# Kernel optimization log

Measured on AMD Instinct MI355X. Metric: run time of the kernel, lower is better.

## Reference

```python
import jax, jax.numpy as jnp
import numpy as np
from jax import lax

# dims
BS, C, H, W = 16, 684, 32, 128   # batch, encoder channels, feature-map H/W
Q, K, PAD = 256, 11, 5           # coverage channels, conv_Q kernel, padding
N, NP = 256, 512                 # decoder hidden n, attention dim n_prime
T = 4                            # prior attention steps stored in alpha


def setup_inputs() -> dict:
    key = jax.random.key(0)
    ks = jax.random.split(key, 10)
    s = 0.02  # small init scale (stand-in for xavier)
    return {
        "x": jax.random.normal(ks[0], (BS, C, H, W), jnp.float32),
        "st_hat": jax.random.normal(ks[1], (BS, 1, N), jnp.float32),
        "alpha": jax.random.uniform(ks[2], (BS, T, H * W), jnp.float32),
        # conv_Q: Conv2d(1, Q, k=11, pad=5)
        "convQ_w": jax.random.normal(ks[3], (Q, 1, K, K), jnp.float32) * s,
        "convQ_b": jnp.zeros((Q,), jnp.float32),
        # fc_Wa: Linear(n, n_prime)
        "Wa_w": jax.random.normal(ks[4], (NP, N), jnp.float32) * s,
        "Wa_b": jnp.zeros((NP,), jnp.float32),
        # conv_Ua: Conv2d(C, n_prime, k=1)
        "convUa_w": jax.random.normal(ks[5], (NP, C, 1, 1), jnp.float32) * s,
        "convUa_b": jnp.zeros((NP,), jnp.float32),
        # fc_Uf: Linear(Q, n_prime)
        "Uf_w": jax.random.normal(ks[6], (NP, Q), jnp.float32) * s,
        "Uf_b": jnp.zeros((NP,), jnp.float32),
        # fc_Va: Linear(n_prime, 1)
        "Va_w": jax.random.normal(ks[7], (1, NP), jnp.float32) * s,
        "Va_b": jnp.zeros((1,), jnp.float32),
    }


def reference(x, st_hat, alpha, convQ_w, convQ_b, Wa_w, Wa_b,
              convUa_w, convUa_b, Uf_w, Uf_b, Va_w, Va_b):
    bs, c, h, w = x.shape
    # beta: sum of past attention maps -> [bs, 1, h, w]
    beta = alpha.sum(axis=1).reshape(bs, 1, h, w)
    # conv_Q: coverage features [bs, Q, h, w]
    Fc = lax.conv_general_dilated(
        beta, convQ_w, window_strides=(1, 1), padding=[(PAD, PAD), (PAD, PAD)],
        dimension_numbers=("NCHW", "OIHW", "NCHW")) + convQ_b[None, :, None, None]
    # fc_Uf over channel dim after permute(2,3,0,1): [h, w, bs, n_prime]
    cover = jnp.einsum("bqhw,pq->hwbp", Fc, Uf_w) + Uf_b
    # conv_Ua (1x1 conv == per-pixel linear): [h, w, bs, n_prime]
    key = jnp.einsum("bchw,pc->hwbp", x, convUa_w[:, :, 0, 0]) + convUa_b
    # fc_Wa(st_hat).squeeze(1): [bs, n_prime]
    query = st_hat[:, 0, :] @ Wa_w.T + Wa_b
    # additive attention score
    score = jnp.tanh(key + query[None, None, :, :] + cover)  # [h,w,bs,np]
    # fc_Va -> e_t, permuted to [bs, h*w] (row-major over h,w like torch view)
    e = jnp.einsum("hwbp,p->bhw", score, Va_w[0]) + Va_b[0]
    e = e.reshape(bs, h * w)
    # softmax with the module's explicit exp/sum + eps formulation
    e_exp = jnp.exp(e)
    alpha_t = e_exp / (e_exp.sum(axis=1, keepdims=True) + 1e-8)  # [bs, hw]
    # context vector g_t = sum_n alpha_t[b,n] * x[b,c,n]
    context = jnp.einsum("bn,bcn->bc", alpha_t, x.reshape(bs, c, h * w))
    return context, alpha_t.reshape(bs, 1, h, w)
```

## Files before the change

### kernel.cpp

```cpp
#include <hip/hip_runtime.h>
#include <math.h>

#define BS 16
#define C_ 684
#define Hh 32
#define Ww 128
#define HW 4096
#define Qc 256
#define NP 512
#define Nn 256
#define NKT 26
#define NB 64

#define WS_BETA 0
#define WS_BIAS 65536
#define WS_EEXP 73728
#define WS_ESUM 139264
#define WS_ASW  139280

typedef __attribute__((ext_vector_type(8))) short bf16x8;
typedef __attribute__((ext_vector_type(4))) float f32x4;

static __device__ __forceinline__ short f2bf(float f) {
    unsigned u = __builtin_bit_cast(unsigned, f);
    u += 0x7fff + ((u >> 16) & 1);
    return (short)(u >> 16);
}

static __device__ __forceinline__ float fast_tanh(float v) {
    float ax = fabsf(v);
    float t = __expf(-2.f * ax);
    float th = (1.f - t) * __builtin_amdgcn_rcpf(1.f + t);
    return copysignf(th, v);
}

__global__ void k_prep(const float* __restrict__ alpha, const float* __restrict__ ua,
                       const float* __restrict__ ufw, const float* __restrict__ qw,
                       const float* __restrict__ st, const float* __restrict__ waw,
                       const float* __restrict__ wab, const float* __restrict__ ufb,
                       const float* __restrict__ qb, const float* __restrict__ uab,
                       float* __restrict__ beta, short* __restrict__ a_sw,
                       float* __restrict__ bias, float* __restrict__ esum) {
    int part = blockIdx.x, tid = threadIdx.x;
    if (part < 256) {
        int idx = part * 256 + tid;
        int b = idx >> 12, n = idx & 4095;
        const float* a = alpha + (size_t)b * 4 * HW + n;
        beta[idx] = a[0] + a[HW] + a[2 * HW] + a[3 * HW];
    } else if (part < 1920) {
        int idx = (part - 256) * 256 + tid;
        int j = idx & 7, m = (idx >> 3) & 511, g = (idx >> 12) & 3, kt = idx >> 14;
        int k = kt * 32 + g * 8 + j;
        float v = 0.f;
        if (k < C_) {
            v = ua[m * C_ + k];
        } else if (k < C_ + 121) {
            int tap = k - C_;
            const float* ur = ufw + m * Qc;
            float s = 0.f;
            for (int q = 0; q < Qc; ++q) s += ur[q] * qw[q * 121 + tap];
            v = s;
        }
        a_sw[idx] = f2bf(v);
    } else if (part < 1952) {
        int idx = (part - 1920) * 256 + tid;
        int b = idx >> 9, p = idx & 511;
        float s = wab[p] + ufb[p] + uab[p];
        const float* sv = st + b * Nn;
        const float* wr = waw + p * Nn;
        for (int n = 0; n < Nn; ++n) s += sv[n] * wr[n];
        const float* ur = ufw + p * Qc;
        for (int q = 0; q < Qc; ++q) s += ur[q] * qb[q];
        bias[idx] = s;
    } else {
        if (tid < BS) esum[tid] = 0.f;
    }
}

__launch_bounds__(256, 2)
__global__ void k_gemm(const short* __restrict__ a_sw, const float* __restrict__ x,
                       const float* __restrict__ beta, const float* __restrict__ bias,
                       const float* __restrict__ vaw, const float* __restrict__ vab,
                       float* __restrict__ eexp, float* __restrict__ esum) {
    __shared__ short Bs[2][4 * NB * 8];
    __shared__ float ered[4][NB];

    const int tid = threadIdx.x;
    const int lane = tid & 63, wid = tid >> 6;
    const int b = blockIdx.y, n0 = blockIdx.x * NB;
    const int q = lane >> 4, r = lane & 15;

    const int sn = tid & 63;
    const int sg = tid >> 6;
    const int n_glob = n0 + sn;
    const int pr = n_glob >> 7, pc = n_glob & 127;
    const float* xb = x + (size_t)b * C_ * HW + n_glob;
    const float* betab = beta + b * HW;

    f32x4 acc[8][4] = {};
    float fv[2][8];

    #define LDSTAGE(KT, DST)                                                  \
    {                                                                         \
        int kbase = (KT) * 32 + sg * 8;                                       \
        _Pragma("unroll")                                                     \
        for (int j = 0; j < 8; ++j) {                                         \
            int k = kbase + j;                                                \
            float f = 0.f;                                                    \
            if (k < C_) {                                                     \
                f = xb[(size_t)k * HW];                                       \
            } else if (k < C_ + 121) {                                        \
                int tap = k - C_;                                             \
                int di = tap / 11, dj = tap - di * 11;                        \
                int rr = pr + di - 5, cc = pc + dj - 5;                       \
                if (rr >= 0 && rr < Hh && cc >= 0 && cc < Ww)                 \
                    f = betab[rr * 128 + cc];                                 \
            }                                                                 \
            (DST)[j] = f;                                                     \
        }                                                                     \
    }

    LDSTAGE(0, fv[0]);
    LDSTAGE(1, fv[1]);

    const short* ap = a_sw + (size_t)(q * NP + wid * 128 + r) * 8;

    #pragma unroll 2
    for (int kt = 0; kt < NKT; ++kt) {
        bf16x8 af[8];
        const short* ak = ap + (size_t)kt * 4 * NP * 8;
        #pragma unroll
        for (int ms = 0; ms < 8; ++ms)
            af[ms] = *(const bf16x8*)(ak + ms * 16 * 8);

        {
            const float* f = fv[kt & 1];
            unsigned pk[4];
            #pragma unroll
            for (int h = 0; h < 4; ++h)
                pk[h] = (unsigned)(unsigned short)f2bf(f[2 * h]) |
                        ((unsigned)(unsigned short)f2bf(f[2 * h + 1]) << 16);
            *(uint4*)&Bs[kt & 1][(sg * NB + sn) * 8] = make_uint4(pk[0], pk[1], pk[2], pk[3]);
        }
        __syncthreads();

        bf16x8 bf[4];
        #pragma unroll
        for (int ns = 0; ns < 4; ++ns)
            bf[ns] = *(const bf16x8*)&Bs[kt & 1][(q * NB + ns * 16 + r) * 8];

        if (kt < NKT - 2) LDSTAGE(kt + 2, fv[kt & 1]);

        #pragma unroll
        for (int ms = 0; ms < 8; ++ms)
            #pragma unroll
            for (int ns = 0; ns < 4; ++ns)
                acc[ms][ns] = __builtin_amdgcn_mfma_f32_16x16x32_bf16(af[ms], bf[ns], acc[ms][ns], 0, 0, 0);
    }
    #undef LDSTAGE

    float es[4] = {0.f, 0.f, 0.f, 0.f};
    #pragma unroll
    for (int ms = 0; ms < 8; ++ms) {
        #pragma unroll
        for (int reg = 0; reg < 4; ++reg) {
            int row = wid * 128 + ms * 16 + q * 4 + reg;
            float bv = bias[b * NP + row];
            float vv = vaw[row];
            #pragma unroll
            for (int ns = 0; ns < 4; ++ns)
                es[ns] += vv * fast_tanh(acc[ms][ns][reg] + bv);
        }
    }
    #pragma unroll
    for (int ns = 0; ns < 4; ++ns) {
        es[ns] += __shfl_xor(es[ns], 16, 64);
        es[ns] += __shfl_xor(es[ns], 32, 64);
    }
    if (lane < 16) {
        #pragma unroll
        for (int ns = 0; ns < 4; ++ns) ered[wid][ns * 16 + r] = es[ns];
    }
    __syncthreads();
    if (tid < NB) {
        float s = ered[0][tid] + ered[1][tid] + ered[2][tid] + ered[3][tid] + vab[0];
        float ex = expf(s);
        eexp[b * HW + n0 + tid] = ex;
        float ps = ex;
        #pragma unroll
        for (int off = 32; off > 0; off >>= 1) ps += __shfl_xor(ps, off, 64);
        if (tid == 0) atomicAdd(&esum[b], ps);
    }
}

__global__ void k_finish(const float* __restrict__ x, const float* __restrict__ eexp,
                         const float* __restrict__ esum, float* __restrict__ ctx,
                         float* __restrict__ aout) {
    int part = blockIdx.x, b = blockIdx.y, tid = threadIdx.x;
    float iv = 1.f / (esum[b] + 1e-8f);
    if (part == 171) {
        for (int k = tid; k < HW; k += 256) aout[b * HW + k] = eexp[b * HW + k] * iv;
        return;
    }
    int wid = tid >> 6, lane = tid & 63;
    int c = part * 4 + wid;
    const float4* xr = (const float4*)(x + ((size_t)b * C_ + c) * HW);
    const float4* er = (const float4*)(eexp + b * HW);
    float acc = 0.f;
    #pragma unroll 8
    for (int k = lane; k < 1024; k += 64) {
        float4 xv = xr[k], ev = er[k];
        acc += xv.x * ev.x + xv.y * ev.y + xv.z * ev.z + xv.w * ev.w;
    }
    #pragma unroll
    for (int off = 32; off > 0; off >>= 1) acc += __shfl_xor(acc, off, 64);
    if (lane == 0) ctx[b * C_ + c] = acc * iv;
}

extern "C" void kernel_launch(void* const* d_in, const int* in_sizes, int n_in,
                              void* d_out, int out_size, void* d_ws, size_t ws_size,
                              hipStream_t stream) {
    const float* x      = (const float*)d_in[0];
    const float* st     = (const float*)d_in[1];
    const float* alpha  = (const float*)d_in[2];
    const float* convQw = (const float*)d_in[3];
    const float* convQb = (const float*)d_in[4];
    const float* Waw    = (const float*)d_in[5];
    const float* Wab    = (const float*)d_in[6];
    const float* Uaw    = (const float*)d_in[7];
    const float* Uab    = (const float*)d_in[8];
    const float* Ufw    = (const float*)d_in[9];
    const float* Ufb    = (const float*)d_in[10];
    const float* Vaw    = (const float*)d_in[11];
    const float* Vab    = (const float*)d_in[12];

    float* ws   = (float*)d_ws;
    float* beta = ws + WS_BETA;
    float* bias = ws + WS_BIAS;
    float* eexp = ws + WS_EEXP;
    float* esum = ws + WS_ESUM;
    short* a_sw = (short*)(ws + WS_ASW);

    float* ctx  = (float*)d_out;
    float* aout = (float*)d_out + BS * C_;

    k_prep<<<1953, 256, 0, stream>>>(alpha, Uaw, Ufw, convQw, st, Waw, Wab, Ufb,
                                     convQb, Uab, beta, a_sw, bias, esum);
    k_gemm<<<dim3(HW / NB, BS), 256, 0, stream>>>(a_sw, x, beta, bias, Vaw, Vab, eexp, esum);
    k_finish<<<dim3(172, BS), 256, 0, stream>>>(x, eexp, esum, ctx, aout);
}
```

Before: 365.0 us.

## Fuse context partial sums into GEMM kernel and add lighter LDS barrier

After computing the exponentiated scores for its 64-pixel tile, each GEMM block immediately multiplies them against the same x tile it just streamed, writing per-tile partial context sums to workspace. A small finish kernel reduces the 64 partials per channel and normalizes, so the separate full re-read of x in the old finish kernel goes away. The in-loop __syncthreads is replaced by an LDS-only waitcnt plus s_barrier so outstanding global prefetches are not drained. The fused path depends on the workspace being large enough and adds partial-sum traffic and a serial per-thread 64-element loop over channels.

```diff
diff --git a/kernel.cpp b/kernel.cpp
--- a/kernel.cpp
+++ b/kernel.cpp
@@ -17,6 +17,7 @@
 #define WS_EEXP 73728
 #define WS_ESUM 139264
 #define WS_ASW  139280
+#define WS_CTXP 352272
 
 typedef __attribute__((ext_vector_type(8))) short bf16x8;
 typedef __attribute__((ext_vector_type(4))) float f32x4;
@@ -77,13 +78,25 @@
     }
 }
 
+#define LIGHT_BARRIER()                                              \
+    do {                                                             \
+        asm volatile("s_waitcnt lgkmcnt(0)" ::: "memory");           \
+        __builtin_amdgcn_sched_barrier(0);                           \
+        __builtin_amdgcn_s_barrier();                                \
+        asm volatile("" ::: "memory");                               \
+        __builtin_amdgcn_sched_barrier(0);                           \
+    } while (0)
+
+template <bool FUSED>
 __launch_bounds__(256, 2)
 __global__ void k_gemm(const short* __restrict__ a_sw, const float* __restrict__ x,
                        const float* __restrict__ beta, const float* __restrict__ bias,
                        const float* __restrict__ vaw, const float* __restrict__ vab,
-                       float* __restrict__ eexp, float* __restrict__ esum) {
+                       float* __restrict__ eexp, float* __restrict__ esum,
+                       float* __restrict__ ctxp) {
     __shared__ short Bs[2][4 * NB * 8];
     __shared__ float ered[4][NB];
+    __shared__ float eeL[NB];
 
     const int tid = threadIdx.x;
     const int lane = tid & 63, wid = tid >> 6;
@@ -142,7 +155,7 @@
                         ((unsigned)(unsigned short)f2bf(f[2 * h + 1]) << 16);
             *(uint4*)&Bs[kt & 1][(sg * NB + sn) * 8] = make_uint4(pk[0], pk[1], pk[2], pk[3]);
         }
-        __syncthreads();
+        LIGHT_BARRIER();
 
         bf16x8 bf[4];
         #pragma unroll
@@ -186,10 +199,25 @@
         float s = ered[0][tid] + ered[1][tid] + ered[2][tid] + ered[3][tid] + vab[0];
         float ex = expf(s);
         eexp[b * HW + n0 + tid] = ex;
+        if (FUSED) eeL[tid] = ex;
         float ps = ex;
         #pragma unroll
         for (int off = 32; off > 0; off >>= 1) ps += __shfl_xor(ps, off, 64);
         if (tid == 0) atomicAdd(&esum[b], ps);
+    }
+
+    if (FUSED) {
+        __syncthreads();
+        for (int c = tid; c < C_; c += 256) {
+            const float* xr = x + ((size_t)b * C_ + c) * HW + n0;
+            float s = 0.f;
+            #pragma unroll
+            for (int n = 0; n < NB; n += 4) {
+                float4 xv = *(const float4*)(xr + n);
+                s += xv.x * eeL[n] + xv.y * eeL[n + 1] + xv.z * eeL[n + 2] + xv.w * eeL[n + 3];
+            }
+            ctxp[((size_t)blockIdx.x * BS + b) * C_ + c] = s;
+        }
     }
 }
 
@@ -215,6 +243,24 @@
     #pragma unroll
     for (int off = 32; off > 0; off >>= 1) acc += __shfl_xor(acc, off, 64);
     if (lane == 0) ctx[b * C_ + c] = acc * iv;
+}
+
+__global__ void k_finish2(const float* __restrict__ eexp, const float* __restrict__ esum,
+                          const float* __restrict__ ctxp, float* __restrict__ ctx,
+                          float* __restrict__ aout) {
+    int part = blockIdx.x, b = blockIdx.y, tid = threadIdx.x;
+    float iv = 1.f / (esum[b] + 1e-8f);
+    int c = part * 171 + tid;
+    if (tid < 171 && c < C_) {
+        float s = 0.f;
+        #pragma unroll 8
+        for (int nb = 0; nb < HW / NB; ++nb)
+            s += ctxp[((size_t)nb * BS + b) * C_ + c];
+        ctx[b * C_ + c] = s * iv;
+    }
+    int k0 = part * 1024;
+    for (int k = tid; k < 1024; k += 256)
+        aout[b * HW + k0 + k] = eexp[b * HW + k0 + k] * iv;
 }
 
 extern "C" void kernel_launch(void* const* d_in, const int* in_sizes, int n_in,
@@ -240,12 +286,23 @@
     float* eexp = ws + WS_EEXP;
     float* esum = ws + WS_ESUM;
     short* a_sw = (short*)(ws + WS_ASW);
+    float* ctxp = ws + WS_CTXP;
 
     float* ctx  = (float*)d_out;
     float* aout = (float*)d_out + BS * C_;
 
+    const size_t ws_need = (size_t)(WS_CTXP + (HW / NB) * BS * C_) * sizeof(float);
+    const bool fused = ws_size >= ws_need;
+
     k_prep<<<1953, 256, 0, stream>>>(alpha, Uaw, Ufw, convQw, st, Waw, Wab, Ufb,
                                      convQb, Uab, beta, a_sw, bias, esum);
-    k_gemm<<<dim3(HW / NB, BS), 256, 0, stream>>>(a_sw, x, beta, bias, Vaw, Vab, eexp, esum);
-    k_finish<<<dim3(172, BS), 256, 0, stream>>>(x, eexp, esum, ctx, aout);
-}
+    if (fused) {
+        k_gemm<true><<<dim3(HW / NB, BS), 256, 0, stream>>>(a_sw, x, beta, bias, Vaw, Vab,
+                                                            eexp, esum, ctxp);
+        k_finish2<<<dim3(4, BS), 256, 0, stream>>>(eexp, esum, ctxp, ctx, aout);
+    } else {
+        k_gemm<false><<<dim3(HW / NB, BS), 256, 0, stream>>>(a_sw, x, beta, bias, Vaw, Vab,
+                                                             eexp, esum, nullptr);
+        k_finish<<<dim3(172, BS), 256, 0, stream>>>(x, eexp, esum, ctx, aout);
+    }
+}
```

After: 356.9 us. -2.2%, faster.

## Fuse context reduction into GEMM epilogue with halved pixel tile

Applied to the files above, without the earlier changes.

Moves the context-vector reduction into the attention GEMM kernel. Each block re-reads its x tile, which is likely still cached, and accumulates unnormalized partial contexts with atomics, so the finish kernel only rescales results. The pixel tile is halved to 32 so more blocks fit, launch bounds rise to 3 blocks per CU, and a lighter barrier plus MFMA priority hints are added. The cost is many more atomic adds, A-fragment reloads for each smaller tile, and a non-deterministic summation order.

```diff
diff --git a/kernel.cpp b/kernel.cpp
--- a/kernel.cpp
+++ b/kernel.cpp
@@ -10,13 +10,14 @@
 #define NP 512
 #define Nn 256
 #define NKT 26
-#define NB 64
+#define NB 32
 
 #define WS_BETA 0
 #define WS_BIAS 65536
 #define WS_EEXP 73728
 #define WS_ESUM 139264
 #define WS_ASW  139280
+#define WS_CTXA 352272
 
 typedef __attribute__((ext_vector_type(8))) short bf16x8;
 typedef __attribute__((ext_vector_type(4))) float f32x4;
@@ -40,7 +41,8 @@
                        const float* __restrict__ wab, const float* __restrict__ ufb,
                        const float* __restrict__ qb, const float* __restrict__ uab,
                        float* __restrict__ beta, short* __restrict__ a_sw,
-                       float* __restrict__ bias, float* __restrict__ esum) {
+                       float* __restrict__ bias, float* __restrict__ esum,
+                       float* __restrict__ ctxa) {
     int part = blockIdx.x, tid = threadIdx.x;
     if (part < 256) {
         int idx = part * 256 + tid;
@@ -74,37 +76,49 @@
         bias[idx] = s;
     } else {
         if (tid < BS) esum[tid] = 0.f;
-    }
-}
-
-__launch_bounds__(256, 2)
+        for (int i = tid; i < BS * C_; i += 256) ctxa[i] = 0.f;
+    }
+}
+
+#define LIGHT_BARRIER()                                              \
+    do {                                                             \
+        asm volatile("s_waitcnt lgkmcnt(0)" ::: "memory");           \
+        __builtin_amdgcn_sched_barrier(0);                           \
+        __builtin_amdgcn_s_barrier();                                \
+        asm volatile("" ::: "memory");                               \
+        __builtin_amdgcn_sched_barrier(0);                           \
+    } while (0)
+
+__launch_bounds__(256, 3)
 __global__ void k_gemm(const short* __restrict__ a_sw, const float* __restrict__ x,
                        const float* __restrict__ beta, const float* __restrict__ bias,
                        const float* __restrict__ vaw, const float* __restrict__ vab,
-                       float* __restrict__ eexp, float* __restrict__ esum) {
+                       float* __restrict__ eexp, float* __restrict__ esum,
+                       float* __restrict__ ctxa) {
     __shared__ short Bs[2][4 * NB * 8];
     __shared__ float ered[4][NB];
+    __shared__ float eeL[NB];
 
     const int tid = threadIdx.x;
     const int lane = tid & 63, wid = tid >> 6;
     const int b = blockIdx.y, n0 = blockIdx.x * NB;
     const int q = lane >> 4, r = lane & 15;
 
-    const int sn = tid & 63;
-    const int sg = tid >> 6;
+    const int sn = tid & 31;
+    const int sg = tid >> 5;
     const int n_glob = n0 + sn;
     const int pr = n_glob >> 7, pc = n_glob & 127;
     const float* xb = x + (size_t)b * C_ * HW + n_glob;
     const float* betab = beta + b * HW;
 
-    f32x4 acc[8][4] = {};
-    float fv[2][8];
+    f32x4 acc[8][2] = {};
+    float fv[2][4];
 
     #define LDSTAGE(KT, DST)                                                  \
     {                                                                         \
-        int kbase = (KT) * 32 + sg * 8;                                       \
+        int kbase = (KT) * 32 + sg * 4;                                       \
         _Pragma("unroll")                                                     \
-        for (int j = 0; j < 8; ++j) {                                         \
+        for (int j = 0; j < 4; ++j) {                                         \
             int k = kbase + j;                                                \
             float f = 0.f;                                                    \
             if (k < C_) {                                                     \
@@ -135,31 +149,33 @@
 
         {
             const float* f = fv[kt & 1];
-            unsigned pk[4];
-            #pragma unroll
-            for (int h = 0; h < 4; ++h)
-                pk[h] = (unsigned)(unsigned short)f2bf(f[2 * h]) |
-                        ((unsigned)(unsigned short)f2bf(f[2 * h + 1]) << 16);
-            *(uint4*)&Bs[kt & 1][(sg * NB + sn) * 8] = make_uint4(pk[0], pk[1], pk[2], pk[3]);
-        }
-        __syncthreads();
-
-        bf16x8 bf[4];
-        #pragma unroll
-        for (int ns = 0; ns < 4; ++ns)
+            unsigned pk0 = (unsigned)(unsigned short)f2bf(f[0]) |
+                           ((unsigned)(unsigned short)f2bf(f[1]) << 16);
+            unsigned pk1 = (unsigned)(unsigned short)f2bf(f[2]) |
+                           ((unsigned)(unsigned short)f2bf(f[3]) << 16);
+            *(uint2*)&Bs[kt & 1][((sg >> 1) * NB + sn) * 8 + (sg & 1) * 4] =
+                make_uint2(pk0, pk1);
+        }
+        LIGHT_BARRIER();
+
+        bf16x8 bf[2];
+        #pragma unroll
+        for (int ns = 0; ns < 2; ++ns)
             bf[ns] = *(const bf16x8*)&Bs[kt & 1][(q * NB + ns * 16 + r) * 8];
 
         if (kt < NKT - 2) LDSTAGE(kt + 2, fv[kt & 1]);
 
+        __builtin_amdgcn_s_setprio(1);
         #pragma unroll
         for (int ms = 0; ms < 8; ++ms)
             #pragma unroll
-            for (int ns = 0; ns < 4; ++ns)
+            for (int ns = 0; ns < 2; ++ns)
                 acc[ms][ns] = __builtin_amdgcn_mfma_f32_16x16x32_bf16(af[ms], bf[ns], acc[ms][ns], 0, 0, 0);
+        __builtin_amdgcn_s_setprio(0);
     }
     #undef LDSTAGE
 
-    float es[4] = {0.f, 0.f, 0.f, 0.f};
+    float es[2] = {0.f, 0.f};
     #pragma unroll
     for (int ms = 0; ms < 8; ++ms) {
         #pragma unroll
@@ -168,53 +184,54 @@
             float bv = bias[b * NP + row];
             float vv = vaw[row];
             #pragma unroll
-            for (int ns = 0; ns < 4; ++ns)
+            for (int ns = 0; ns < 2; ++ns)
                 es[ns] += vv * fast_tanh(acc[ms][ns][reg] + bv);
         }
     }
     #pragma unroll
-    for (int ns = 0; ns < 4; ++ns) {
+    for (int ns = 0; ns < 2; ++ns) {
         es[ns] += __shfl_xor(es[ns], 16, 64);
         es[ns] += __shfl_xor(es[ns], 32, 64);
     }
     if (lane < 16) {
         #pragma unroll
-        for (int ns = 0; ns < 4; ++ns) ered[wid][ns * 16 + r] = es[ns];
+        for (int ns = 0; ns < 2; ++ns) ered[wid][ns * 16 + r] = es[ns];
     }
     __syncthreads();
     if (tid < NB) {
         float s = ered[0][tid] + ered[1][tid] + ered[2][tid] + ered[3][tid] + vab[0];
         float ex = expf(s);
         eexp[b * HW + n0 + tid] = ex;
+        eeL[tid] = ex;
         float ps = ex;
         #pragma unroll
-        for (int off = 32; off > 0; off >>= 1) ps += __shfl_xor(ps, off, 64);
+        for (int off = 16; off > 0; off >>= 1) ps += __shfl_xor(ps, off, 32);
         if (tid == 0) atomicAdd(&esum[b], ps);
     }
-}
-
-__global__ void k_finish(const float* __restrict__ x, const float* __restrict__ eexp,
-                         const float* __restrict__ esum, float* __restrict__ ctx,
+    __syncthreads();
+
+    for (int c = tid; c < C_; c += 256) {
+        const float* xr = x + ((size_t)b * C_ + c) * HW + n0;
+        float s = 0.f;
+        #pragma unroll
+        for (int n = 0; n < NB; n += 4) {
+            float4 xv = *(const float4*)(xr + n);
+            s += xv.x * eeL[n] + xv.y * eeL[n + 1] + xv.z * eeL[n + 2] + xv.w * eeL[n + 3];
+        }
+        atomicAdd(&ctxa[b * C_ + c], s);
+    }
+}
+
+__global__ void k_finish(const float* __restrict__ eexp, const float* __restrict__ esum,
+                         const float* __restrict__ ctxa, float* __restrict__ ctx,
                          float* __restrict__ aout) {
     int part = blockIdx.x, b = blockIdx.y, tid = threadIdx.x;
     float iv = 1.f / (esum[b] + 1e-8f);
-    if (part == 171) {
-        for (int k = tid; k < HW; k += 256) aout[b * HW + k] = eexp[b * HW + k] * iv;
-        return;
-    }
-    int wid = tid >> 6, lane = tid & 63;
-    int c = part * 4 + wid;
-    const float4* xr = (const float4*)(x + ((size_t)b * C_ + c) * HW);
-    const float4* er = (const float4*)(eexp + b * HW);
-    float acc = 0.f;
-    #pragma unroll 8
-    for (int k = lane; k < 1024; k += 64) {
-        float4 xv = xr[k], ev = er[k];
-        acc += xv.x * ev.x + xv.y * ev.y + xv.z * ev.z + xv.w * ev.w;
-    }
-    #pragma unroll
-    for (int off = 32; off > 0; off >>= 1) acc += __shfl_xor(acc, off, 64);
-    if (lane == 0) ctx[b * C_ + c] = acc * iv;
+    int c = part * 171 + tid;
+    if (tid < 171 && c < C_) ctx[b * C_ + c] = ctxa[b * C_ + c] * iv;
+    int k0 = part * 1024;
+    for (int k = tid; k < 1024; k += 256)
+        aout[b * HW + k0 + k] = eexp[b * HW + k0 + k] * iv;
 }
 
 extern "C" void kernel_launch(void* const* d_in, const int* in_sizes, int n_in,
@@ -240,12 +257,14 @@
     float* eexp = ws + WS_EEXP;
     float* esum = ws + WS_ESUM;
     short* a_sw = (short*)(ws + WS_ASW);
+    float* ctxa = ws + WS_CTXA;
 
     float* ctx  = (float*)d_out;
     float* aout = (float*)d_out + BS * C_;
 
     k_prep<<<1953, 256, 0, stream>>>(alpha, Uaw, Ufw, convQw, st, Waw, Wab, Ufb,
-                                     convQb, Uab, beta, a_sw, bias, esum);
-    k_gemm<<<dim3(HW / NB, BS), 256, 0, stream>>>(a_sw, x, beta, bias, Vaw, Vab, eexp, esum);
-    k_finish<<<dim3(172, BS), 256, 0, stream>>>(x, eexp, esum, ctx, aout);
-}
+                                     convQb, Uab, beta, a_sw, bias, esum, ctxa);
+    k_gemm<<<dim3(HW / NB, BS), 256, 0, stream>>>(a_sw, x, beta, bias, Vaw, Vab,
+                                                  eexp, esum, ctxa);
+    k_finish<<<dim3(4, BS), 256, 0, stream>>>(eexp, esum, ctxa, ctx, aout);
+}
```

Result: slower. 443.3 us (+21.4%).
